# Optimization experiments

Hardware: AMD Instinct MI355X
Metric: run time of the kernel (lower is better)

The kernel has to match this reference:

```python
import jax, jax.numpy as jnp
import numpy as np

B, C, N, K = 4, 64, 8192, 16
OUT = 128

def setup_inputs() -> dict:
    key = jax.random.key(0)
    k1, k2, k3, k4 = jax.random.split(key, 4)
    x = jax.random.normal(k1, (B, C, N, 1), dtype=jnp.float32)
    edge_index = jax.random.randint(k2, (2, B, N, K), 0, N)
    # BasicConv([2C, OUT]) is a 1x1 Conv2d -> weight [OUT, 2C], bias [OUT]
    W_nn = jax.random.normal(k3, (OUT, 2 * C), dtype=jnp.float32) * 0.02
    b_nn = jax.random.normal(k4, (OUT,), dtype=jnp.float32) * 0.02
    return {"x": x, "edge_index": edge_index, "W_nn": W_nn, "b_nn": b_nn}

def _gather_nodes(x2, idx):
    # x2: [B, C, N], idx: [B, N, K] -> [B, C, N, K]
    return jax.vmap(lambda xb, ib: xb[:, ib])(x2, idx)

def reference(x, edge_index, W_nn, b_nn):
    b, c, n, _ = x.shape
    x2 = x[:, :, :, 0]                      # [B, C, N]
    x_i = _gather_nodes(x2, edge_index[1])  # [B, C, N, K]
    x_j = _gather_nodes(x2, edge_index[0])  # [B, C, N, K]
    x_j = jnp.max(x_j - x_i, axis=-1, keepdims=True)  # [B, C, N, 1]
    # interleave channels: cat([x.unsqueeze(2), x_j.unsqueeze(2)], dim=2).reshape(b, 2c, n, 1)
    h = jnp.concatenate([x[:, :, None], x_j[:, :, None]], axis=2).reshape(b, 2 * c, n, 1)
    # BasicConv: 1x1 conv + bias + ReLU
    out = jnp.einsum('oc,bcn->bon', W_nn, h[:, :, :, 0]) + b_nn[None, :, None]
    return jax.nn.relu(out)[:, :, :, None]  # [B, OUT, N, 1]
```

## Files before the change

kernel.cpp:

```cpp
#include <hip/hip_runtime.h>
#include <cstddef>

#define BB 4
#define CC 64
#define NN 8192
#define KK 16
#define OO 128

#define SW 136
#define SH 136

typedef __attribute__((ext_vector_type(8))) short bf16x8;
typedef __attribute__((ext_vector_type(4))) float f32x4;

__device__ __forceinline__ unsigned short f2b(float f) {
    unsigned u = __builtin_bit_cast(unsigned, f);
    unsigned r = (u + 0x7fffu + ((u >> 16) & 1u)) >> 16;
    return (unsigned short)r;
}

__device__ __forceinline__ float b2f(unsigned short h) {
    unsigned u = ((unsigned)h) << 16;
    return __builtin_bit_cast(float, u);
}

__global__ __launch_bounds__(256) void transpose_kernel(
        const float* __restrict__ x, unsigned short* __restrict__ xt) {
    __shared__ float tile[64][65];
    const int b  = blockIdx.y;
    const int n0 = blockIdx.x * 64;
    const int t  = threadIdx.x;
    const int ln = t & 63;
    const int r  = t >> 6;

    const float* xb = x + (size_t)b * CC * NN;
    #pragma unroll
    for (int s = 0; s < 64; s += 4) {
        int c = s + r;
        tile[c][ln] = xb[(size_t)c * NN + n0 + ln];
    }
    __syncthreads();
    unsigned short* xtb = xt + ((size_t)b * NN + n0) * CC;
    #pragma unroll
    for (int s = 0; s < 64; s += 4) {
        int n = s + r;
        xtb[n * CC + ln] = f2b(tile[ln][n]);
    }
}

__global__ __launch_bounds__(256) void main_kernel(
        const unsigned short* __restrict__ xt,
        const int*            __restrict__ eidx,
        const float*          __restrict__ W,
        const float*          __restrict__ bias,
        float*                __restrict__ out) {
    __shared__ unsigned short Wl[128 * SW];
    __shared__ unsigned short hl[64 * SH];

    const int t    = threadIdx.x;
    const int lane = t & 63;
    const int w    = t >> 6;
    const int b    = blockIdx.y;
    const int n_base = blockIdx.x * 64;

    #pragma unroll
    for (int s = 0; s < 16384; s += 1024) {
        int idx = s + t * 4;
        float4 v = *reinterpret_cast<const float4*>(W + idx);
        int row = idx >> 7;
        int col = idx & 127;
        unsigned short* dst = &Wl[row * SW + col];
        dst[0] = f2b(v.x); dst[1] = f2b(v.y); dst[2] = f2b(v.z); dst[3] = f2b(v.w);
    }

    const unsigned short* xtb = xt + (size_t)b * NN * CC;
    const int* e0 = eidx + (size_t)b * NN * KK;
    const int* e1 = e0 + (size_t)BB * NN * KK;
    const int c = lane;

    for (int nn = 0; nn < 16; nn++) {
        int nl = w * 16 + nn;
        int n_u = __builtin_amdgcn_readfirstlane(n_base + nl);
        const int* p0 = e0 + (size_t)n_u * KK;
        const int* p1 = e1 + (size_t)n_u * KK;

        float xv = b2f(xtb[(size_t)n_u * CC + c]);
        float m = -1e30f;
        #pragma unroll
        for (int k = 0; k < KK; k++) {
            int j = p0[k];
            int i = p1[k];
            float xj = b2f(xtb[(size_t)j * CC + c]);
            float xi = b2f(xtb[(size_t)i * CC + c]);
            m = fmaxf(m, xj - xi);
        }
        unsigned pk = (unsigned)f2b(xv) | ((unsigned)f2b(m) << 16);
        *reinterpret_cast<unsigned*>(&hl[nl * SH + 2 * c]) = pk;
    }
    __syncthreads();

    const int quad = lane >> 4;
    const int l15  = lane & 15;
    const int o0w  = w * 32;

    bf16x8 afr[2][4];
    #pragma unroll
    for (int ot = 0; ot < 2; ot++)
        #pragma unroll
        for (int ks = 0; ks < 4; ks++) {
            const unsigned short* ap = &Wl[(o0w + ot * 16 + l15) * SW + ks * 32 + quad * 8];
            afr[ot][ks] = *reinterpret_cast<const bf16x8*>(ap);
        }

    #pragma unroll
    for (int nt = 0; nt < 4; nt++) {
        f32x4 acc0 = {0.f, 0.f, 0.f, 0.f};
        f32x4 acc1 = {0.f, 0.f, 0.f, 0.f};
        #pragma unroll
        for (int ks = 0; ks < 4; ks++) {
            const unsigned short* bp = &hl[(nt * 16 + l15) * SH + ks * 32 + quad * 8];
            bf16x8 bfr = *reinterpret_cast<const bf16x8*>(bp);
            acc0 = __builtin_amdgcn_mfma_f32_16x16x32_bf16(afr[0][ks], bfr, acc0, 0, 0, 0);
            acc1 = __builtin_amdgcn_mfma_f32_16x16x32_bf16(afr[1][ks], bfr, acc1, 0, 0, 0);
        }
        int n_g = n_base + nt * 16 + l15;
        #pragma unroll
        for (int r = 0; r < 4; r++) {
            int o_a = o0w + quad * 4 + r;
            int o_b = o0w + 16 + quad * 4 + r;
            float va = acc0[r] + bias[o_a];
            float vb = acc1[r] + bias[o_b];
            out[((size_t)b * OO + o_a) * NN + n_g] = fmaxf(va, 0.f);
            out[((size_t)b * OO + o_b) * NN + n_g] = fmaxf(vb, 0.f);
        }
    }
}

extern "C" void kernel_launch(void* const* d_in, const int* in_sizes, int n_in,
                              void* d_out, int out_size, void* d_ws, size_t ws_size,
                              hipStream_t stream) {
    const float* x    = (const float*)d_in[0];
    const int*   eidx = (const int*)d_in[1];
    const float* W    = (const float*)d_in[2];
    const float* bias = (const float*)d_in[3];
    float* out = (float*)d_out;
    unsigned short* xt = (unsigned short*)d_ws;

    dim3 blk(256);
    dim3 grid(NN / 64, BB);
    transpose_kernel<<<grid, blk, 0, stream>>>(x, xt);
    main_kernel<<<grid, blk, 0, stream>>>(xt, eidx, W, bias, out);
}
```

Before: 92.45 us.

## Vectorize neighbor gathers, stage edge indices in LDS, precompute bf16 weights

The gather phase changes from one channel per lane with scalar 2-byte loads to 8 lanes per node, each loading 16-byte chunks (8 bf16 channels) per neighbor. Each wave now handles 8 nodes at a time, and the edge indices for the block's 64 nodes are loaded into LDS once with vectorized loads. Weights are converted to bf16 once in the transpose kernel and copied into LDS with 16-byte loads, so each block no longer converts W itself. The intent is to cut the number of memory transactions and scalar index loads. The cost is more registers per lane and an extra workspace buffer.

Result: faster. 83.21 us (-10.0%).

```diff
diff --git a/kernel.cpp b/kernel.cpp
--- a/kernel.cpp
+++ b/kernel.cpp
@@ -19,13 +19,16 @@
     return (unsigned short)r;
 }
 
-__device__ __forceinline__ float b2f(unsigned short h) {
-    unsigned u = ((unsigned)h) << 16;
-    return __builtin_bit_cast(float, u);
+__device__ __forceinline__ float bclo(unsigned d) {
+    return __builtin_bit_cast(float, d << 16);
+}
+__device__ __forceinline__ float bchi(unsigned d) {
+    return __builtin_bit_cast(float, d & 0xffff0000u);
 }
 
 __global__ __launch_bounds__(256) void transpose_kernel(
-        const float* __restrict__ x, unsigned short* __restrict__ xt) {
+        const float* __restrict__ x, unsigned short* __restrict__ xt,
+        const float* __restrict__ W, unsigned short* __restrict__ Wbf) {
     __shared__ float tile[64][65];
     const int b  = blockIdx.y;
     const int n0 = blockIdx.x * 64;
@@ -46,16 +49,25 @@
         int n = s + r;
         xtb[n * CC + ln] = f2b(tile[ln][n]);
     }
+
+    if (b == 0 && blockIdx.x < 16) {
+        int idx = blockIdx.x * 1024 + t * 4;
+        float4 v = *reinterpret_cast<const float4*>(W + idx);
+        ushort4 o;
+        o.x = f2b(v.x); o.y = f2b(v.y); o.z = f2b(v.z); o.w = f2b(v.w);
+        *reinterpret_cast<ushort4*>(Wbf + idx) = o;
+    }
 }
 
 __global__ __launch_bounds__(256) void main_kernel(
         const unsigned short* __restrict__ xt,
+        const unsigned short* __restrict__ Wbf,
         const int*            __restrict__ eidx,
-        const float*          __restrict__ W,
         const float*          __restrict__ bias,
         float*                __restrict__ out) {
     __shared__ unsigned short Wl[128 * SW];
     __shared__ unsigned short hl[64 * SH];
+    __shared__ int eL[2048];
 
     const int t    = threadIdx.x;
     const int lane = t & 63;
@@ -63,39 +75,65 @@
     const int b    = blockIdx.y;
     const int n_base = blockIdx.x * 64;
 
+    const int* e0 = eidx + ((size_t)b * NN + n_base) * KK;
+    const int* e1 = e0 + (size_t)BB * NN * KK;
+    *reinterpret_cast<int4*>(&eL[t * 4])        = *reinterpret_cast<const int4*>(e0 + t * 4);
+    *reinterpret_cast<int4*>(&eL[1024 + t * 4]) = *reinterpret_cast<const int4*>(e1 + t * 4);
+
     #pragma unroll
-    for (int s = 0; s < 16384; s += 1024) {
-        int idx = s + t * 4;
-        float4 v = *reinterpret_cast<const float4*>(W + idx);
-        int row = idx >> 7;
-        int col = idx & 127;
-        unsigned short* dst = &Wl[row * SW + col];
-        dst[0] = f2b(v.x); dst[1] = f2b(v.y); dst[2] = f2b(v.z); dst[3] = f2b(v.w);
+    for (int it = 0; it < 8; it++) {
+        int flat = it * 2048 + t * 8;
+        int row = flat >> 7, col = flat & 127;
+        *reinterpret_cast<int4*>(&Wl[row * SW + col]) =
+            *reinterpret_cast<const int4*>(Wbf + flat);
     }
+    __syncthreads();
 
     const unsigned short* xtb = xt + (size_t)b * NN * CC;
-    const int* e0 = eidx + (size_t)b * NN * KK;
-    const int* e1 = e0 + (size_t)BB * NN * KK;
-    const int c = lane;
+    const int g = lane >> 3;
+    const int p = lane & 7;
 
-    for (int nn = 0; nn < 16; nn++) {
-        int nl = w * 16 + nn;
-        int n_u = __builtin_amdgcn_readfirstlane(n_base + nl);
-        const int* p0 = e0 + (size_t)n_u * KK;
-        const int* p1 = e1 + (size_t)n_u * KK;
+    #pragma unroll
+    for (int bt = 0; bt < 2; bt++) {
+        const int nl = w * 16 + bt * 8 + g;
+        uint4 xr = *reinterpret_cast<const uint4*>(xtb + (size_t)(n_base + nl) * CC + p * 8);
 
-        float xv = b2f(xtb[(size_t)n_u * CC + c]);
-        float m = -1e30f;
+        float m[8];
+        #pragma unroll
+        for (int j = 0; j < 8; j++) m[j] = -1e30f;
+
         #pragma unroll
         for (int k = 0; k < KK; k++) {
-            int j = p0[k];
-            int i = p1[k];
-            float xj = b2f(xtb[(size_t)j * CC + c]);
-            float xi = b2f(xtb[(size_t)i * CC + c]);
-            m = fmaxf(m, xj - xi);
+            int ij = eL[nl * KK + k];
+            int ii = eL[1024 + nl * KK + k];
+            uint4 xj = *reinterpret_cast<const uint4*>(xtb + (size_t)ij * CC + p * 8);
+            uint4 xi = *reinterpret_cast<const uint4*>(xtb + (size_t)ii * CC + p * 8);
+            m[0] = fmaxf(m[0], bclo(xj.x) - bclo(xi.x));
+            m[1] = fmaxf(m[1], bchi(xj.x) - bchi(xi.x));
+            m[2] = fmaxf(m[2], bclo(xj.y) - bclo(xi.y));
+            m[3] = fmaxf(m[3], bchi(xj.y) - bchi(xi.y));
+            m[4] = fmaxf(m[4], bclo(xj.z) - bclo(xi.z));
+            m[5] = fmaxf(m[5], bchi(xj.z) - bchi(xi.z));
+            m[6] = fmaxf(m[6], bclo(xj.w) - bclo(xi.w));
+            m[7] = fmaxf(m[7], bchi(xj.w) - bchi(xi.w));
         }
-        unsigned pk = (unsigned)f2b(xv) | ((unsigned)f2b(m) << 16);
-        *reinterpret_cast<unsigned*>(&hl[nl * SH + 2 * c]) = pk;
+
+        unsigned xs[8];
+        xs[0] = xr.x & 0xffffu; xs[1] = xr.x >> 16;
+        xs[2] = xr.y & 0xffffu; xs[3] = xr.y >> 16;
+        xs[4] = xr.z & 0xffffu; xs[5] = xr.z >> 16;
+        xs[6] = xr.w & 0xffffu; xs[7] = xr.w >> 16;
+        unsigned od[8];
+        #pragma unroll
+        for (int j = 0; j < 8; j++)
+            od[j] = xs[j] | ((unsigned)f2b(m[j]) << 16);
+
+        unsigned short* dst = &hl[nl * SH + p * 16];
+        uint4 lo, hi;
+        lo.x = od[0]; lo.y = od[1]; lo.z = od[2]; lo.w = od[3];
+        hi.x = od[4]; hi.y = od[5]; hi.z = od[6]; hi.w = od[7];
+        *reinterpret_cast<uint4*>(dst)     = lo;
+        *reinterpret_cast<uint4*>(dst + 8) = hi;
     }
     __syncthreads();
 
@@ -144,10 +182,12 @@
     const float* W    = (const float*)d_in[2];
     const float* bias = (const float*)d_in[3];
     float* out = (float*)d_out;
-    unsigned short* xt = (unsigned short*)d_ws;
+
+    unsigned short* xt  = (unsigned short*)d_ws;
+    unsigned short* Wbf = (unsigned short*)((char*)d_ws + 4 * 1024 * 1024);
 
     dim3 blk(256);
     dim3 grid(NN / 64, BB);
-    transpose_kernel<<<grid, blk, 0, stream>>>(x, xt);
-    main_kernel<<<grid, blk, 0, stream>>>(xt, eidx, W, bias, out);
+    transpose_kernel<<<grid, blk, 0, stream>>>(x, xt, W, Wbf);
+    main_kernel<<<grid, blk, 0, stream>>>(xt, Wbf, eidx, bias, out);
 }
```
